# Optimization experiments

Measured on AMD Instinct MI355X. Metric: run time of the kernel, lower is better.

The kernel has to match this reference:

```python
import jax, jax.numpy as jnp
import numpy as np

N_NODES = 50000
N_EDGES = 1600000
D_IN = 128
D_HID = 256


def gcn_conv(x, edge_index, W, b, n_nodes):
    # PyG GCNConv: linear transform, add self-loops, symmetric deg^-1/2 normalization,
    # scatter-sum aggregation, then bias.
    h = x @ W                                             # [N, out]
    src, dst = edge_index[0], edge_index[1]
    loop = jnp.arange(n_nodes, dtype=src.dtype)
    src = jnp.concatenate([src, loop])
    dst = jnp.concatenate([dst, loop])
    deg = jax.ops.segment_sum(jnp.ones_like(dst, x.dtype), dst, num_segments=n_nodes)
    dinv = jnp.where(deg > 0, jax.lax.rsqrt(deg), 0.0)    # deg^-1/2, guard isolated nodes
    norm = dinv[src] * dinv[dst]                          # [E+N]
    msg = norm[:, None] * h[src]                          # gather + scale
    out = jax.ops.segment_sum(msg, dst, num_segments=n_nodes)  # scatter-sum
    return out + b


def setup_inputs() -> dict:
    key = jax.random.key(0)
    k_x, k_e, k_w1, k_b1, k_w2, k_b2 = jax.random.split(key, 6)
    x = jax.random.normal(k_x, (N_NODES, D_IN), dtype=jnp.float32)
    edge_index = jax.random.randint(k_e, (2, N_EDGES), 0, N_NODES, dtype=jnp.int64)
    s = 1.0 / np.sqrt(D_IN)
    W1 = jax.random.uniform(k_w1, (D_IN, D_HID), jnp.float32, -s, s)
    b1 = jnp.zeros((D_HID,), jnp.float32)
    s2 = 1.0 / np.sqrt(D_HID)
    W2 = jax.random.uniform(k_w2, (D_HID, D_IN), jnp.float32, -s2, s2)
    b2 = jnp.zeros((D_IN,), jnp.float32)
    return {"x": x, "edge_index": edge_index, "W1": W1, "b1": b1, "W2": W2, "b2": b2}


def reference(x, edge_index, W1, b1, W2, b2):
    h = gcn_conv(x, edge_index, W1, b1, N_NODES)   # conv1 (hetero sum over 1 edge type)
    h = jax.nn.relu(h)
    out = gcn_conv(h, edge_index, W2, b2, N_NODES) # conv2 -> x_dict['asset']
    return out
```

## Files before the change

kernel.cpp:

```cpp
#include <hip/hip_runtime.h>

#define N_NODES 50000
#define N_EDGES 1600000
#define D_IN 128
#define D_HID 256

#define NBKT 196
#define BCAP 12288
#define CHUNK 4096

typedef short bh8 __attribute__((ext_vector_type(8)));
typedef float f32x4 __attribute__((ext_vector_type(4)));

__device__ inline unsigned int f2_to_bf16x2(float a, float b) {
    unsigned int ua = __float_as_uint(a);
    ua = (ua + 0x7FFFu + ((ua >> 16) & 1u)) >> 16;
    unsigned int ub = __float_as_uint(b);
    ub = (ub + 0x7FFFu + ((ub >> 16) & 1u)) >> 16;
    return ua | (ub << 16);
}
__device__ inline unsigned short f_to_bf16(float a) {
    unsigned int ua = __float_as_uint(a);
    return (unsigned short)((ua + 0x7FFFu + ((ua >> 16) & 1u)) >> 16);
}
__device__ inline float2 bf16x2_to_f2(unsigned int p) {
    float2 r;
    r.x = __uint_as_float(p << 16);
    r.y = __uint_as_float(p & 0xFFFF0000u);
    return r;
}

__global__ __launch_bounds__(256) void bin_kernel(
        const int* __restrict__ src, const int* __restrict__ dst,
        int* __restrict__ bcur, unsigned int* __restrict__ binned, int E) {
    __shared__ unsigned int staged[CHUNK];
    __shared__ unsigned int sorted[CHUNK];
    __shared__ int hist[NBKT], lbase[NBKT], gbase[NBKT];
    __shared__ int sc[256];
    const int tid = threadIdx.x;
    if (tid < NBKT) hist[tid] = 0;
    __syncthreads();
    const int cbase = blockIdx.x * CHUNK;
    const int n = min(CHUNK, E - cbase);
    for (int i = tid; i < n; i += 256) {
        int s = src[cbase + i], d = dst[cbase + i];
        staged[i] = ((unsigned)s << 16) | (unsigned)d;
        atomicAdd(&hist[d >> 8], 1);
    }
    __syncthreads();
    int h = (tid < NBKT) ? hist[tid] : 0;
    sc[tid] = h;
    __syncthreads();
    for (int off = 1; off < 256; off <<= 1) {
        int a = (tid >= off) ? sc[tid - off] : 0;
        __syncthreads();
        sc[tid] += a;
        __syncthreads();
    }
    if (tid < NBKT) {
        lbase[tid] = sc[tid] - h;
        gbase[tid] = h ? atomicAdd(&bcur[tid], h) : 0;
        hist[tid] = 0;
    }
    __syncthreads();
    for (int i = tid; i < n; i += 256) {
        unsigned r = staged[i];
        int b = (r & 0xFFFF) >> 8;
        sorted[lbase[b] + atomicAdd(&hist[b], 1)] = r;
    }
    __syncthreads();
    for (int j = tid; j < n; j += 256) {
        unsigned r = sorted[j];
        int b = (r & 0xFFFF) >> 8;
        binned[(size_t)b * BCAP + gbase[b] + (j - lbase[b])] = r;
    }
}

__global__ __launch_bounds__(256) void scanB(const int* __restrict__ bcur,
                                             int* __restrict__ brow) {
    __shared__ int sc[256];
    const int tid = threadIdx.x;
    int v = (tid < NBKT) ? bcur[tid] : 0;
    sc[tid] = v;
    __syncthreads();
    for (int off = 1; off < 256; off <<= 1) {
        int a = (tid >= off) ? sc[tid - off] : 0;
        __syncthreads();
        sc[tid] += a;
        __syncthreads();
    }
    if (tid < NBKT) brow[tid] = sc[tid] - v;
}

__global__ __launch_bounds__(256) void count_kernel(
        const unsigned int* __restrict__ binned, const int* __restrict__ bcur,
        const int* __restrict__ brow, int* __restrict__ deg,
        float* __restrict__ dinv, int* __restrict__ rowptr, int nNodes) {
    __shared__ int h[256], sc[256];
    const int b = blockIdx.x, tid = threadIdx.x;
    h[tid] = 0;
    __syncthreads();
    const int cnt = bcur[b];
    for (int j = tid; j < cnt; j += 256)
        atomicAdd(&h[binned[(size_t)b * BCAP + j] & 0xFF], 1);
    __syncthreads();
    int d0 = h[tid];
    sc[tid] = d0;
    __syncthreads();
    for (int off = 1; off < 256; off <<= 1) {
        int a = (tid >= off) ? sc[tid - off] : 0;
        __syncthreads();
        sc[tid] += a;
        __syncthreads();
    }
    int node = b * 256 + tid;
    if (node < nNodes) {
        deg[node] = d0;
        dinv[node] = rsqrtf((float)(d0 + 1));
        rowptr[node] = brow[b] + sc[tid] - d0;
    }
}

__global__ __launch_bounds__(256) void place_kernel(
        const unsigned int* __restrict__ binned, const int* __restrict__ bcur,
        const int* __restrict__ rowptr, const float* __restrict__ dinv,
        unsigned short* __restrict__ eS, float* __restrict__ eW, int nNodes) {
    __shared__ int cur[256];
    __shared__ float sdinv[256];
    __shared__ unsigned short recS[BCAP];
    const int b = blockIdx.x, tid = threadIdx.x;
    const int nbase = b * 256;
    const int regionBase = rowptr[nbase];
    int node = nbase + tid;
    cur[tid] = (node < nNodes) ? (rowptr[node] - regionBase) : 0;
    sdinv[tid] = (node < nNodes) ? dinv[node] : 0.0f;
    __syncthreads();
    int cnt = bcur[b];
    if (cnt <= BCAP) {
        for (int j = tid; j < cnt; j += 256) {
            unsigned r = binned[(size_t)b * BCAP + j];
            int dl = r & 0xFF;
            int s = r >> 16;
            int p = atomicAdd(&cur[dl], 1);
            recS[p] = (unsigned short)s;
            eW[regionBase + p] = dinv[s] * sdinv[dl];
        }
        __syncthreads();
        for (int j = tid; j < cnt; j += 256)
            eS[regionBase + j] = recS[j];
    } else {
        for (int j = tid; j < cnt; j += 256) {
            unsigned r = binned[(size_t)b * BCAP + j];
            int dl = r & 0xFF;
            int s = r >> 16;
            int p = atomicAdd(&cur[dl], 1);
            eS[regionBase + p] = (unsigned short)s;
            eW[regionBase + p] = dinv[s] * sdinv[dl];
        }
    }
}

__global__ __launch_bounds__(256) void cvt_bf16(const float4* __restrict__ in,
                                                uint2* __restrict__ out, int n4) {
    int i = blockIdx.x * blockDim.x + threadIdx.x;
    if (i < n4) {
        float4 v = in[i];
        out[i] = make_uint2(f2_to_bf16x2(v.x, v.y), f2_to_bf16x2(v.z, v.w));
    }
}

__global__ __launch_bounds__(256) void cvtT_both(const float* __restrict__ W1,
                                                 const float* __restrict__ W2,
                                                 unsigned short* __restrict__ W1T,
                                                 unsigned short* __restrict__ W2T) {
    int t = blockIdx.x * blockDim.x + threadIdx.x;
    const int SZ = D_IN * D_HID;
    if (t < SZ) {
        int n = t / D_IN, k = t - n * D_IN;
        W1T[t] = f_to_bf16(W1[(size_t)k * D_HID + n]);
    } else if (t < 2 * SZ) {
        int u = t - SZ;
        int n = u / D_HID, k = u - n * D_HID;
        W2T[u] = f_to_bf16(W2[(size_t)k * D_IN + n]);
    }
}

template<bool OUT_BF16>
__global__ __launch_bounds__(256) void gather_agg_bf16(
        const unsigned int* __restrict__ hb,
        const unsigned short* __restrict__ eS,
        const float* __restrict__ eW,
        const int* __restrict__ rowptr, const int* __restrict__ deg,
        const float* __restrict__ dinv, const float* __restrict__ bias,
        void* __restrict__ out, int n) {
    int lane = threadIdx.x & 63;
    int node = blockIdx.x * 4 + (threadIdx.x >> 6);
    if (node >= n) return;
    int start = rowptr[node];
    int cnt = deg[node];
    float dn = dinv[node];
    float2 hv = bf16x2_to_f2(hb[(size_t)node * 64 + lane]);
    float2 acc = make_float2(dn * dn * hv.x, dn * dn * hv.y);
    for (int c0 = 0; c0 < cnt; c0 += 64) {
        int m = min(64, cnt - c0);
        int   es = (lane < m) ? (int)eS[start + c0 + lane] : 0;
        float ws = (lane < m) ? eW[start + c0 + lane] : 0.0f;
        int mr = (m + 7) & ~7;
        for (int j = 0; j < mr; j += 8) {
            float2 vv[8];
            float ww[8];
            #pragma unroll
            for (int k = 0; k < 8; ++k) {
                int sj = __shfl(es, j + k);
                ww[k] = __shfl(ws, j + k);
                vv[k] = bf16x2_to_f2(hb[(size_t)sj * 64 + lane]);
            }
            #pragma unroll
            for (int k = 0; k < 8; ++k) {
                acc.x += ww[k] * vv[k].x;
                acc.y += ww[k] * vv[k].y;
            }
        }
    }
    if (OUT_BF16) {
        ((unsigned int*)out)[(size_t)node * 64 + lane] = f2_to_bf16x2(acc.x, acc.y);
    } else {
        float2 b = ((const float2*)bias)[lane];
        acc.x += b.x;
        acc.y += b.y;
        ((float2*)((float*)out + (size_t)node * D_IN))[lane] = acc;
    }
}

template<int N, int K, int MODE>
__global__ __launch_bounds__(256) void gemm_mfma(
        const unsigned short* __restrict__ WT,
        const unsigned int* __restrict__ Ab,
        const float* __restrict__ bias,
        unsigned short* __restrict__ Cb,
        int M) {
    constexpr int KP = K + 8;
    constexpr int KSTEPS = K / 32;
    constexpr int TPW = N / 64;
    __shared__ unsigned short Bs[N * KP];

    const int tid = threadIdx.x;
    for (int c = tid; c < N * (K / 8); c += 256) {
        int nn = c / (K / 8), kc = c - nn * (K / 8);
        uint4 v = ((const uint4*)(WT + (size_t)nn * K))[kc];
        *(uint4*)&Bs[nn * KP + kc * 8] = v;
    }
    __syncthreads();

    const int wave = tid >> 6, lane = tid & 63;
    const int n0 = wave * (TPW * 16);
    const int m_base = blockIdx.x * 128;
    const int rit = lane & 15;
    const int kg = lane >> 4;

    f32x4 acc[8][TPW];
    #pragma unroll
    for (int rg = 0; rg < 8; ++rg)
        #pragma unroll
        for (int t = 0; t < TPW; ++t)
            acc[rg][t] = (f32x4){0.f, 0.f, 0.f, 0.f};

    bh8 a0[8], a1[8];
    #define LOAD_A(KS, DST)                                                  \
        _Pragma("unroll")                                                    \
        for (int rg = 0; rg < 8; ++rg) {                                     \
            int m = m_base + rg * 16 + rit;                                  \
            m = min(m, M - 1);                                               \
            DST[rg] = *(const bh8*)(Ab + (size_t)m * (K / 2) + (KS)*16 + kg * 4); \
        }

    LOAD_A(0, a0)
    #pragma unroll
    for (int ks = 0; ks < KSTEPS; ++ks) {
        if (ks + 1 < KSTEPS) {
            if ((ks & 1) == 0) { LOAD_A(ks + 1, a1) }
            else               { LOAD_A(ks + 1, a0) }
        }
        #pragma unroll
        for (int t = 0; t < TPW; ++t) {
            bh8 b = *(const bh8*)&Bs[(n0 + t * 16 + rit) * KP + ks * 32 + kg * 8];
            #pragma unroll
            for (int rg = 0; rg < 8; ++rg) {
                bh8 a = ((ks & 1) == 0) ? a0[rg] : a1[rg];
                acc[rg][t] = __builtin_amdgcn_mfma_f32_16x16x32_bf16(
                    a, b, acc[rg][t], 0, 0, 0);
            }
        }
    }
    #undef LOAD_A

    #pragma unroll
    for (int t = 0; t < TPW; ++t) {
        int col = n0 + t * 16 + rit;
        float bv = (MODE == 1) ? bias[col] : 0.0f;
        #pragma unroll
        for (int rg = 0; rg < 8; ++rg) {
            #pragma unroll
            for (int i = 0; i < 4; ++i) {
                int m = m_base + rg * 16 + kg * 4 + i;
                float v = acc[rg][t][i];
                if (MODE == 1) { v += bv; v = fmaxf(v, 0.0f); }
                if (m < M) Cb[(size_t)m * N + col] = f_to_bf16(v);
            }
        }
    }
}

extern "C" void kernel_launch(void* const* d_in, const int* in_sizes, int n_in,
                              void* d_out, int out_size, void* d_ws, size_t ws_size,
                              hipStream_t stream) {
    const float* x  = (const float*)d_in[0];
    const int*   ei = (const int*)d_in[1];
    const float* W1 = (const float*)d_in[2];
    const float* b1 = (const float*)d_in[3];
    const float* W2 = (const float*)d_in[4];
    const float* b2 = (const float*)d_in[5];
    const int* src = ei;
    const int* dst = ei + N_EDGES;
    float* out = (float*)d_out;

    char* ws = (char*)d_ws;
    size_t off = 0;
    auto carve = [&](size_t bytes) {
        char* p = ws + off;
        off += (bytes + 255) & ~size_t(255);
        return p;
    };
    int*   bcur      = (int*)  carve(256 * sizeof(int));
    int*   brow      = (int*)  carve(256 * sizeof(int));
    int*   deg       = (int*)  carve(N_NODES * sizeof(int));
    int*   rowptr    = (int*)  carve(N_NODES * sizeof(int));
    float* dinv      = (float*)carve(N_NODES * sizeof(float));
    unsigned int*   binned = (unsigned int*)  carve((size_t)NBKT * BCAP * sizeof(unsigned int));
    unsigned short* eS     = (unsigned short*)carve((size_t)N_EDGES * sizeof(unsigned short));
    float*          eWt    = (float*)         carve((size_t)N_EDGES * sizeof(float));
    unsigned int* xb   = (unsigned int*)carve((size_t)N_NODES * 64 * sizeof(unsigned int));
    unsigned int* aggb = (unsigned int*)carve((size_t)N_NODES * 64 * sizeof(unsigned int));
    unsigned int* h1b  = (unsigned int*)carve((size_t)N_NODES * 128 * sizeof(unsigned int));
    unsigned short* W1T = (unsigned short*)carve((size_t)D_IN * D_HID * sizeof(unsigned short));
    unsigned short* W2T = (unsigned short*)carve((size_t)D_HID * D_IN * sizeof(unsigned short));
    unsigned int* t2b = xb;
    (void)ws_size;

    hipMemsetAsync(bcur, 0, 256 * sizeof(int), stream);
    bin_kernel<<<(N_EDGES + CHUNK - 1) / CHUNK, 256, 0, stream>>>(
        src, dst, bcur, binned, N_EDGES);
    scanB<<<1, 256, 0, stream>>>(bcur, brow);
    count_kernel<<<NBKT, 256, 0, stream>>>(binned, bcur, brow, deg, dinv,
                                           rowptr, N_NODES);
    place_kernel<<<NBKT, 256, 0, stream>>>(binned, bcur, rowptr, dinv,
                                           eS, eWt, N_NODES);

    cvt_bf16<<<(N_NODES * D_IN / 4 + 255) / 256, 256, 0, stream>>>(
        (const float4*)x, (uint2*)xb, N_NODES * D_IN / 4);
    cvtT_both<<<(2 * D_IN * D_HID + 255) / 256, 256, 0, stream>>>(W1, W2, W1T, W2T);

    gather_agg_bf16<true><<<(N_NODES + 3) / 4, 256, 0, stream>>>(
        xb, eS, eWt, rowptr, deg, dinv, nullptr, (void*)aggb, N_NODES);

    gemm_mfma<D_HID, D_IN, 1><<<(N_NODES + 127) / 128, 256, 0, stream>>>(
        W1T, aggb, b1, (unsigned short*)h1b, N_NODES);

    gemm_mfma<D_IN, D_HID, 2><<<(N_NODES + 127) / 128, 256, 0, stream>>>(
        W2T, h1b, nullptr, (unsigned short*)t2b, N_NODES);

    gather_agg_bf16<false><<<(N_NODES + 3) / 4, 256, 0, stream>>>(
        t2b, eS, eWt, rowptr, deg, dinv, b2, (void*)out, N_NODES);
}
```

Before: 311.6 us.

## Replace LDS-staged GEMM with per-wave register-resident weight tiles

Both dense GEMMs are restructured so each wavefront owns a 128-row by 16*TPW-column output tile and loads its weight slice straight from global memory into registers, with no shared-memory staging and no block barrier. This removes the per-block copy of the full weight matrix into LDS and its sync, and launches many more waves so the MFMA units stay busier. In exchange the A rows are re-read from global/L2 once per column group, which multiplies activation traffic, and the weight fragments held in registers may lower occupancy.

```diff
diff --git a/kernel.cpp b/kernel.cpp
--- a/kernel.cpp
+++ b/kernel.cpp
@@ -232,79 +232,59 @@
     }
 }
 
-template<int N, int K, int MODE>
-__global__ __launch_bounds__(256) void gemm_mfma(
+template<int N, int K, int TPW, int MODE>
+__global__ __launch_bounds__(256) void gemm_mfma_ws(
         const unsigned short* __restrict__ WT,
         const unsigned int* __restrict__ Ab,
         const float* __restrict__ bias,
         unsigned short* __restrict__ Cb,
         int M) {
-    constexpr int KP = K + 8;
     constexpr int KSTEPS = K / 32;
-    constexpr int TPW = N / 64;
-    __shared__ unsigned short Bs[N * KP];
-
-    const int tid = threadIdx.x;
-    for (int c = tid; c < N * (K / 8); c += 256) {
-        int nn = c / (K / 8), kc = c - nn * (K / 8);
-        uint4 v = ((const uint4*)(WT + (size_t)nn * K))[kc];
-        *(uint4*)&Bs[nn * KP + kc * 8] = v;
-    }
-    __syncthreads();
-
-    const int wave = tid >> 6, lane = tid & 63;
-    const int n0 = wave * (TPW * 16);
-    const int m_base = blockIdx.x * 128;
+    constexpr int NTG = N / (16 * TPW);
+    const int gw = (blockIdx.x * 256 + threadIdx.x) >> 6;
+    const int lane = threadIdx.x & 63;
+    const int mb = gw / NTG;
+    const int ng = gw - mb * NTG;
+    const int m_base = mb * 128;
+    if (m_base >= M) return;
     const int rit = lane & 15;
     const int kg = lane >> 4;
 
-    f32x4 acc[8][TPW];
-    #pragma unroll
-    for (int rg = 0; rg < 8; ++rg)
-        #pragma unroll
-        for (int t = 0; t < TPW; ++t)
-            acc[rg][t] = (f32x4){0.f, 0.f, 0.f, 0.f};
-
-    bh8 a0[8], a1[8];
-    #define LOAD_A(KS, DST)                                                  \
-        _Pragma("unroll")                                                    \
-        for (int rg = 0; rg < 8; ++rg) {                                     \
-            int m = m_base + rg * 16 + rit;                                  \
-            m = min(m, M - 1);                                               \
-            DST[rg] = *(const bh8*)(Ab + (size_t)m * (K / 2) + (KS)*16 + kg * 4); \
-        }
-
-    LOAD_A(0, a0)
-    #pragma unroll
-    for (int ks = 0; ks < KSTEPS; ++ks) {
-        if (ks + 1 < KSTEPS) {
-            if ((ks & 1) == 0) { LOAD_A(ks + 1, a1) }
-            else               { LOAD_A(ks + 1, a0) }
-        }
-        #pragma unroll
-        for (int t = 0; t < TPW; ++t) {
-            bh8 b = *(const bh8*)&Bs[(n0 + t * 16 + rit) * KP + ks * 32 + kg * 8];
-            #pragma unroll
-            for (int rg = 0; rg < 8; ++rg) {
-                bh8 a = ((ks & 1) == 0) ? a0[rg] : a1[rg];
-                acc[rg][t] = __builtin_amdgcn_mfma_f32_16x16x32_bf16(
-                    a, b, acc[rg][t], 0, 0, 0);
-            }
-        }
-    }
-    #undef LOAD_A
-
+    bh8 b[TPW][KSTEPS];
+    float bv[TPW];
     #pragma unroll
     for (int t = 0; t < TPW; ++t) {
-        int col = n0 + t * 16 + rit;
-        float bv = (MODE == 1) ? bias[col] : 0.0f;
-        #pragma unroll
-        for (int rg = 0; rg < 8; ++rg) {
+        const int col = (ng * TPW + t) * 16 + rit;
+        #pragma unroll
+        for (int ks = 0; ks < KSTEPS; ++ks)
+            b[t][ks] = *(const bh8*)(WT + (size_t)col * K + ks * 32 + kg * 8);
+        bv[t] = (MODE == 1) ? bias[col] : 0.0f;
+    }
+
+    #pragma unroll
+    for (int rg = 0; rg < 8; ++rg) {
+        const int mr = min(m_base + rg * 16 + rit, M - 1);
+        bh8 a[KSTEPS];
+        #pragma unroll
+        for (int ks = 0; ks < KSTEPS; ++ks)
+            a[ks] = *(const bh8*)(Ab + (size_t)mr * (K / 2) + ks * 16 + kg * 4);
+        f32x4 acc[TPW];
+        #pragma unroll
+        for (int t = 0; t < TPW; ++t) acc[t] = (f32x4){0.f, 0.f, 0.f, 0.f};
+        #pragma unroll
+        for (int ks = 0; ks < KSTEPS; ++ks)
+            #pragma unroll
+            for (int t = 0; t < TPW; ++t)
+                acc[t] = __builtin_amdgcn_mfma_f32_16x16x32_bf16(
+                    a[ks], b[t][ks], acc[t], 0, 0, 0);
+        #pragma unroll
+        for (int t = 0; t < TPW; ++t) {
+            const int col = (ng * TPW + t) * 16 + rit;
             #pragma unroll
             for (int i = 0; i < 4; ++i) {
-                int m = m_base + rg * 16 + kg * 4 + i;
-                float v = acc[rg][t][i];
-                if (MODE == 1) { v += bv; v = fmaxf(v, 0.0f); }
+                const int m = m_base + rg * 16 + kg * 4 + i;
+                float v = acc[t][i];
+                if (MODE == 1) { v += bv[t]; v = fmaxf(v, 0.0f); }
                 if (m < M) Cb[(size_t)m * N + col] = f_to_bf16(v);
             }
         }
@@ -363,11 +343,19 @@
     gather_agg_bf16<true><<<(N_NODES + 3) / 4, 256, 0, stream>>>(
         xb, eS, eWt, rowptr, deg, dinv, nullptr, (void*)aggb, N_NODES);
 
-    gemm_mfma<D_HID, D_IN, 1><<<(N_NODES + 127) / 128, 256, 0, stream>>>(
-        W1T, aggb, b1, (unsigned short*)h1b, N_NODES);
-
-    gemm_mfma<D_IN, D_HID, 2><<<(N_NODES + 127) / 128, 256, 0, stream>>>(
-        W2T, h1b, nullptr, (unsigned short*)t2b, N_NODES);
+    const int mB = (N_NODES + 127) / 128;
+
+    {
+        const int waves = mB * (D_HID / 32);
+        gemm_mfma_ws<D_HID, D_IN, 2, 1><<<(waves + 3) / 4, 256, 0, stream>>>(
+            W1T, aggb, b1, (unsigned short*)h1b, N_NODES);
+    }
+
+    {
+        const int waves = mB * (D_IN / 16);
+        gemm_mfma_ws<D_IN, D_HID, 1, 2><<<(waves + 3) / 4, 256, 0, stream>>>(
+            W2T, h1b, nullptr, (unsigned short*)t2b, N_NODES);
+    }
 
     gather_agg_bf16<false><<<(N_NODES + 3) / 4, 256, 0, stream>>>(
         t2b, eS, eWt, rowptr, deg, dinv, b2, (void*)out, N_NODES);
```

After: 293.9 us. 1.06x faster.
